# Performance work log

Measured on AMD Instinct MI355X. Metric: run time of the kernel, lower is better.

Reference implementation:

```python
import jax, jax.numpy as jnp
import numpy as np

VIOL_TOL = 12.0
CLASH_TOL = 1.5
C_N_LEN = (1.329, 1.341)        # (non-proline, proline)
C_N_STD = (0.014, 0.016)
CA_C_N = (-0.5203, 0.0353)      # (gt cos, stddev)
C_N_CA = (-0.4473, 0.0311)
EPS = 1e-6


def setup_inputs() -> dict:
    key = jax.random.key(0)
    k = jax.random.split(key, 6)
    B, N = 1, 512
    pos = jax.random.normal(k[0], (B, N, 14, 3), jnp.float32) * 5.0
    atom_mask = jnp.ones((B, N, 14), jnp.float32)
    residue_types = jax.random.randint(k[1], (B, N), 0, 21, dtype=jnp.int32)
    residue_index = jnp.broadcast_to(jnp.arange(N, dtype=jnp.int32)[None], (B, N))
    vdw_table = jax.random.uniform(k[2], (21, 14), jnp.float32, 1.0, 2.0)
    lower_bound_table = jax.random.uniform(k[3], (21, 14, 14), jnp.float32, 1.0, 2.0)
    upper_bound_table = lower_bound_table + jax.random.uniform(k[4], (21, 14, 14), jnp.float32, 0.5, 1.5)
    return {
        'predicted_positions': pos,
        'atom_mask': atom_mask,
        'residue_types': residue_types,
        'residue_index': residue_index,
        'vdw_table': vdw_table,
        'lower_bound_table': lower_bound_table,
        'upper_bound_table': upper_bound_table,
    }


def _bond_angle_losses(pos, atom_mask, residue_types, residue_index):
    f32 = pos.dtype
    this_ca, this_ca_m = pos[:, :-1, 1, :], atom_mask[:, :-1, 1]
    this_c, this_c_m = pos[:, :-1, 2, :], atom_mask[:, :-1, 2]
    next_n, next_n_m = pos[:, 1:, 0, :], atom_mask[:, 1:, 0]
    next_ca, next_ca_m = pos[:, 1:, 1, :], atom_mask[:, 1:, 1]
    no_gap = (residue_index[:, 1:] - residue_index[:, :-1] == 1).astype(f32)

    c_n_len = jnp.sqrt(jnp.sum((this_c - next_n) ** 2, -1) + EPS)
    pro = (residue_types[:, 1:] == 14).astype(f32)
    gt_len = (1.0 - pro) * C_N_LEN[0] + pro * C_N_LEN[1]
    gt_std = (1.0 - pro) * C_N_STD[0] + pro * C_N_STD[1]
    c_n_mask = this_c_m * next_n_m * no_gap
    c_n_err = jnp.sqrt((c_n_len - gt_len) ** 2 + EPS)
    c_n_loss = jnp.sum(c_n_mask * jax.nn.relu(c_n_err - VIOL_TOL * gt_std), -1) / (jnp.sum(c_n_mask, -1) + EPS)

    ca_c_len = jnp.sqrt(jnp.sum((this_ca - this_c) ** 2, -1) + EPS)
    n_ca_len = jnp.sqrt(jnp.sum((next_n - next_ca) ** 2, -1) + EPS)
    c_ca_u = (this_ca - this_c) / ca_c_len[..., None]
    c_n_u = (next_n - this_c) / c_n_len[..., None]
    n_ca_u = (next_ca - next_n) / n_ca_len[..., None]

    ca_c_n = jnp.sum(c_ca_u * c_n_u, -1)
    ca_c_n_mask = this_ca_m * this_c_m * next_n_m * no_gap
    ca_c_n_err = jnp.sqrt((ca_c_n - CA_C_N[0]) ** 2 + EPS)
    ca_c_n_loss = jnp.sum(ca_c_n_mask * jax.nn.relu(ca_c_n_err - VIOL_TOL * CA_C_N[1]), -1) / (jnp.sum(ca_c_n_mask, -1) + EPS)

    c_n_ca = jnp.sum(-c_n_u * n_ca_u, -1)
    c_n_ca_mask = this_c_m * next_n_m * next_ca_m * no_gap
    c_n_ca_err = jnp.sqrt((c_n_ca - C_N_CA[0]) ** 2 + EPS)
    c_n_ca_loss = jnp.sum(c_n_ca_mask * jax.nn.relu(c_n_ca_err - VIOL_TOL * C_N_CA[1]), -1) / (jnp.sum(c_n_ca_mask, -1) + EPS)

    return c_n_loss, ca_c_n_loss, c_n_ca_loss


def _clash_per_atom(pos, atom_mask, residue_types, residue_index, vdw_table):
    f32 = pos.dtype
    B, N = pos.shape[:2]
    A = N * 14
    pos_f = pos.reshape(B, A, 3)
    m_f = atom_mask.reshape(B, A)
    rt = jnp.minimum(residue_types, 20)
    vdw_f = vdw_table[rt].reshape(B, A)  # gather [B,N,14] -> flat

    diff = pos_f[:, :, None, :] - pos_f[:, None, :, :]
    dist = jnp.sqrt(jnp.sum(diff ** 2, -1) + 1e-8)  # [B,A,A]

    pair = m_f[:, :, None] * m_f[:, None, :]
    ari = jnp.repeat(residue_index, 14, axis=1)  # atom residue index [B,A]
    pair = pair * (ari[:, :, None] < ari[:, None, :]).astype(f32)

    slot = jnp.tile(jnp.arange(14), N)[None]  # [1,A]
    rtf = jnp.repeat(residue_types, 14, axis=1)
    c_n_bond = ((slot[:, :, None] == 2) & (slot[:, None, :] == 0) & (ari[:, None, :] - ari[:, :, None] == 1)) | \
               ((slot[:, :, None] == 0) & (slot[:, None, :] == 2) & (ari[:, :, None] - ari[:, None, :] == 1))
    disulfide = (rtf[:, :, None] == 4) & (rtf[:, None, :] == 4) & (slot[:, :, None] == 5) & (slot[:, None, :] == 5)
    pair = pair * (~c_n_bond).astype(f32) * (~disulfide).astype(f32)

    vdw_sum = vdw_f[:, :, None] + vdw_f[:, None, :]
    clash = jax.nn.relu(vdw_sum - CLASH_TOL - dist) * pair
    per_atom = (jnp.sum(clash, axis=1) + jnp.sum(clash, axis=2)).reshape(B, N, 14)
    return per_atom


def _within_per_atom(pos, atom_mask, residue_types, lower_bound_table, upper_bound_table):
    f32 = pos.dtype
    rt = jnp.minimum(residue_types, 20)
    lb = lower_bound_table[rt]  # [B,N,14,14]
    ub = upper_bound_table[rt]
    d = jnp.sqrt(jnp.sum((pos[:, :, :, None, :] - pos[:, :, None, :, :]) ** 2, -1) + 1e-8)
    pair = atom_mask[:, :, :, None] * atom_mask[:, :, None, :]
    pair = pair * (1.0 - jnp.eye(14, dtype=f32)[None, None])
    pair = pair * ((lb > 0.0) | (ub > 0.0)).astype(f32)
    loss = (jax.nn.relu(lb - d) + jax.nn.relu(d - ub)) * pair
    return jnp.sum(loss, axis=-2) + jnp.sum(loss, axis=-1)  # [B,N,14]


def reference(predicted_positions, atom_mask, residue_types, residue_index,
              vdw_table, lower_bound_table, upper_bound_table):
    c_n, ca_c_n, c_n_ca = _bond_angle_losses(predicted_positions, atom_mask, residue_types, residue_index)
    clash_pa = _clash_per_atom(predicted_positions, atom_mask, residue_types, residue_index, vdw_table)
    within_pa = _within_per_atom(predicted_positions, atom_mask, residue_types, lower_bound_table, upper_bound_table)
    num_atoms = jnp.clip(jnp.sum(atom_mask, axis=(1, 2)), 1e-6, None)
    clash_loss = jnp.sum(clash_pa + within_pa, axis=(1, 2)) / num_atoms
    return c_n + ca_c_n + c_n_ca + clash_loss
```

## Files before the change

### kernel.cpp

```cpp
#include <hip/hip_runtime.h>

#define EPS 1e-6f
#define JT 128
#define WB 64

static __device__ __forceinline__ float wave_reduce_add(float v) {
#pragma unroll
    for (int o = 32; o > 0; o >>= 1) v += __shfl_down(v, o, 64);
    return v;
}


__device__ void do_bonds(const float* __restrict__ P, const float* __restrict__ M,
                         const int* __restrict__ RT, const int* __restrict__ RI,
                         float* __restrict__ W, int N) {
    float n0 = 0.f, de0 = 0.f, n1 = 0.f, de1 = 0.f, n2 = 0.f, de2 = 0.f;
    for (int i = threadIdx.x; i < N - 1; i += blockDim.x) {
        float no_gap = (RI[i + 1] - RI[i] == 1) ? 1.f : 0.f;
        const float* ca0 = P + i * 42 + 3;
        const float* c0  = P + i * 42 + 6;
        const float* nn  = P + (i + 1) * 42 + 0;
        const float* ca1 = P + (i + 1) * 42 + 3;
        float m_ca0 = M[i * 14 + 1], m_c0 = M[i * 14 + 2];
        float m_nn = M[(i + 1) * 14 + 0], m_ca1 = M[(i + 1) * 14 + 1];

        float bx = nn[0] - c0[0], by = nn[1] - c0[1], bz = nn[2] - c0[2];
        float c_n_len = sqrtf(bx * bx + by * by + bz * bz + EPS);
        float pro = (RT[i + 1] == 14) ? 1.f : 0.f;
        float gt_len = (1.f - pro) * 1.329f + pro * 1.341f;
        float gt_std = (1.f - pro) * 0.014f + pro * 0.016f;
        float cnm = m_c0 * m_nn * no_gap;
        float dl = c_n_len - gt_len;
        float cne = sqrtf(dl * dl + EPS);
        n0 += cnm * fmaxf(cne - 12.f * gt_std, 0.f);
        de0 += cnm;

        float ax = ca0[0] - c0[0], ay = ca0[1] - c0[1], az = ca0[2] - c0[2];
        float ca_c_len = sqrtf(ax * ax + ay * ay + az * az + EPS);
        float ex = ca1[0] - nn[0], ey = ca1[1] - nn[1], ez = ca1[2] - nn[2];
        float n_ca_len = sqrtf(ex * ex + ey * ey + ez * ez + EPS);
        float inv_cn = 1.f / c_n_len, inv_ac = 1.f / ca_c_len, inv_nc = 1.f / n_ca_len;
        float ux = bx * inv_cn, uy = by * inv_cn, uz = bz * inv_cn;
        float cx = ax * inv_ac, cy = ay * inv_ac, cz = az * inv_ac;
        float wx = ex * inv_nc, wy = ey * inv_nc, wz = ez * inv_nc;

        float cacn = cx * ux + cy * uy + cz * uz;
        float m1 = m_ca0 * m_c0 * m_nn * no_gap;
        float t1 = cacn + 0.5203f;
        float e1 = sqrtf(t1 * t1 + EPS);
        n1 += m1 * fmaxf(e1 - 12.f * 0.0353f, 0.f);
        de1 += m1;

        float cnca = -(ux * wx + uy * wy + uz * wz);
        float m2 = m_c0 * m_nn * m_ca1 * no_gap;
        float t2 = cnca + 0.4473f;
        float e2 = sqrtf(t2 * t2 + EPS);
        n2 += m2 * fmaxf(e2 - 12.f * 0.0311f, 0.f);
        de2 += m2;
    }
    n0 = wave_reduce_add(n0); de0 = wave_reduce_add(de0);
    n1 = wave_reduce_add(n1); de1 = wave_reduce_add(de1);
    n2 = wave_reduce_add(n2); de2 = wave_reduce_add(de2);
    __shared__ float red[12];
    int lane = threadIdx.x & 63, wid = threadIdx.x >> 6;
    if (lane == 0) {
        red[wid * 6 + 0] = n0; red[wid * 6 + 1] = de0; red[wid * 6 + 2] = n1;
        red[wid * 6 + 3] = de1; red[wid * 6 + 4] = n2; red[wid * 6 + 5] = de2;
    }
    __syncthreads();
    if (threadIdx.x == 0) {
        atomicAdd(&W[0], red[0] + red[6]); atomicAdd(&W[1], red[1] + red[7]);
        atomicAdd(&W[2], red[2] + red[8]); atomicAdd(&W[3], red[3] + red[9]);
        atomicAdd(&W[4], red[4] + red[10]); atomicAdd(&W[5], red[5] + red[11]);
    }
}

__device__ void do_within(const float* __restrict__ pos, const float* __restrict__ am,
                          const int* __restrict__ rtypes,
                          const float* __restrict__ lbt, const float* __restrict__ ubt,
                          float* __restrict__ W, int N, int b, int wblk) {
    int total = N * 196;
    float sum = 0.f;
    for (int idx = wblk * blockDim.x + threadIdx.x; idx < total; idx += WB * blockDim.x) {
        int n = idx / 196;
        int p = idx - n * 196;
        int i = p / 14;
        int j = p - i * 14;
        if (i == j) continue;
        size_t bn = (size_t)b * N + n;
        int rt = rtypes[bn]; rt = rt < 20 ? rt : 20;
        const float* pi = pos + bn * 42 + i * 3;
        const float* pj = pos + bn * 42 + j * 3;
        float dx = pi[0] - pj[0], dy = pi[1] - pj[1], dz = pi[2] - pj[2];
        float d = sqrtf(dx * dx + dy * dy + dz * dz + 1e-8f);
        float lb = lbt[rt * 196 + p], ub = ubt[rt * 196 + p];
        float gate = (lb > 0.f || ub > 0.f) ? 1.f : 0.f;
        float m = am[bn * 14 + i] * am[bn * 14 + j] * gate;
        sum += (fmaxf(lb - d, 0.f) + fmaxf(d - ub, 0.f)) * m;
    }
    sum = wave_reduce_add(sum);
    __shared__ float red2[2];
    int lane = threadIdx.x & 63, wid = threadIdx.x >> 6;
    if (lane == 0) red2[wid] = sum;
    __syncthreads();
    if (threadIdx.x == 0) {
        float s = red2[0] + red2[1];
        if (s != 0.f) atomicAdd(&W[7], s);
    }
}

__device__ void do_clash(const float* __restrict__ P, const float* __restrict__ M,
                         const int* __restrict__ RT, const int* __restrict__ RI,
                         const float* __restrict__ vdw, float* __restrict__ W,
                         int N, int A, int T, int p) {
    int bi = (int)floorf(((float)(2 * T + 1)
                - sqrtf((float)((2 * T + 1) * (2 * T + 1) - 8 * p))) * 0.5f);
    bi = bi < 0 ? 0 : (bi >= T ? T - 1 : bi);
    while (bi + 1 <= T - 1 && ((bi + 1) * T - (bi + 1) * bi / 2) <= p) ++bi;
    while ((bi * T - bi * (bi - 1) / 2) > p) --bi;
    int bj = bi + (p - (bi * T - bi * (bi - 1) / 2));

    __shared__ float4 sPos[JT];
    __shared__ float sMask[JT];
    __shared__ int sRI[JT];
    __shared__ int sMeta[JT];

    int t = threadIdx.x;
    int j = bj * JT + t;
    if (j < A) {
        int res = j / 14;
        int sl = j - res * 14;
        int rt = RT[res];
        int rtc = rt < 20 ? rt : 20;
        sPos[t] = make_float4(P[j * 3], P[j * 3 + 1], P[j * 3 + 2], vdw[rtc * 14 + sl]);
        sMask[t] = M[j];
        sRI[t] = RI[res];
        sMeta[t] = sl | (((rt == 4) && (sl == 5)) ? 16 : 0);
    } else {
        sPos[t] = make_float4(1e30f, 1e30f, 1e30f, -1e30f);
        sMask[t] = 0.f; sRI[t] = 0x7fffffff; sMeta[t] = 0;
    }
    __syncthreads();

    int i = bi * JT + t;
    float sum = 0.f;
    if (i < A) {
        int res = i / 14;
        int isl = i - res * 14;
        int irt = RT[res];
        int rtc = irt < 20 ? irt : 20;
        float vis = vdw[rtc * 14 + isl] - 1.5f;
        float xi = P[i * 3], yi = P[i * 3 + 1], zi = P[i * 3 + 2];
        float mi = M[i];
        int iri = RI[res];
        bool icys = (irt == 4) && (isl == 5);
        if (mi != 0.f) {
            for (int base = 0; base < JT; base += 8) {
                float4 r[8];
#pragma unroll
                for (int k = 0; k < 8; ++k) r[k] = sPos[base + k];
#pragma unroll
                for (int k = 0; k < 8; ++k) {
                    float dx = xi - r[k].x, dy = yi - r[k].y, dz = zi - r[k].z;
                    float d2 = dx * dx + dy * dy + dz * dz + 1e-8f;
                    float s = vis + r[k].w;
                    if (d2 < s * s && s > 0.f) {
                        int jj = base + k;
                        int jg = bj * JT + jj;
                        if (i < jg) {
                            int jri = sRI[jj];
                            if (iri != jri) {
                                int dj = jri - iri;
                                int jmeta = sMeta[jj];
                                int jsl = jmeta & 15;
                                bool cn = (isl == 2 && jsl == 0 && dj == 1) ||
                                          (isl == 0 && jsl == 2 && dj == -1);
                                bool ssb = icys && (jmeta & 16);
                                if (!cn && !ssb) {
                                    sum += (s - sqrtf(d2)) * mi * sMask[jj];
                                }
                            }
                        }
                    }
                }
            }
        }
    }
    sum = wave_reduce_add(sum);
    __shared__ float red3[2];
    int lane = t & 63, wid = t >> 6;
    if (lane == 0) red3[wid] = sum;
    __syncthreads();
    if (t == 0) {
        float s = red3[0] + red3[1];
        if (s != 0.f) atomicAdd(&W[6], s);
    }
}

__global__ __launch_bounds__(JT) void main_kernel(
        const float* __restrict__ pos, const float* __restrict__ am,
        const int* __restrict__ rtypes, const int* __restrict__ rindex,
        const float* __restrict__ vdw, const float* __restrict__ lbt,
        const float* __restrict__ ubt, float* __restrict__ ws,
        int N, int A, int T, int CB) {
    int b = blockIdx.y;
    const float* P = pos + (size_t)b * A * 3;
    const float* M = am + (size_t)b * A;
    const int* RT = rtypes + (size_t)b * N;
    const int* RI = rindex + (size_t)b * N;
    float* W = ws + b * 8;
    int bid = blockIdx.x;
    if (bid < CB) {
        do_clash(P, M, RT, RI, vdw, W, N, A, T, bid);
    } else if (bid < CB + WB) {
        do_within(pos, am, rtypes, lbt, ubt, W, N, b, bid - CB);
    } else {
        do_bonds(P, M, RT, RI, W, N);
    }
}

__global__ __launch_bounds__(128) void final_kernel(
        const float* __restrict__ am, const float* __restrict__ ws,
        float* __restrict__ out, int N) {
    int b = blockIdx.x;
    const float* M = am + (size_t)b * N * 14;
    float s = 0.f;
    for (int i = threadIdx.x; i < N * 14; i += blockDim.x) s += M[i];
    s = wave_reduce_add(s);
    __shared__ float red[2];
    int lane = threadIdx.x & 63, wid = threadIdx.x >> 6;
    if (lane == 0) red[wid] = s;
    __syncthreads();
    if (threadIdx.x == 0) {
        float na = fmaxf(red[0] + red[1], 1e-6f);
        const float* W = ws + b * 8;
        float loss = W[0] / (W[1] + EPS) + W[2] / (W[3] + EPS) + W[4] / (W[5] + EPS)
                   + 2.f * (W[6] + W[7]) / na;
        out[b] = loss;
    }
}

extern "C" void kernel_launch(void* const* d_in, const int* in_sizes, int n_in,
                              void* d_out, int out_size, void* d_ws, size_t ws_size,
                              hipStream_t stream) {
    const float* pos = (const float*)d_in[0];
    const float* am = (const float*)d_in[1];
    const int* rtypes = (const int*)d_in[2];
    const int* rindex = (const int*)d_in[3];
    const float* vdw = (const float*)d_in[4];
    const float* lbt = (const float*)d_in[5];
    const float* ubt = (const float*)d_in[6];
    float* out = (float*)d_out;
    float* ws = (float*)d_ws;

    int B = out_size;
    int N = in_sizes[2] / B;
    int A = N * 14;
    int T = (A + JT - 1) / JT;
    int CB = T * (T + 1) / 2;

    hipMemsetAsync(ws, 0, (size_t)B * 8 * sizeof(float), stream);
    dim3 grid(CB + WB + 1, B);
    main_kernel<<<grid, JT, 0, stream>>>(pos, am, rtypes, rindex, vdw, lbt, ubt,
                                         ws, N, A, T, CB);
    final_kernel<<<B, 128, 0, stream>>>(am, ws, out, N);
}
```

Baseline: 106.0 us.

## Replace atomics and memset with per-block partial slots; enlarge clash tiles to 256

Each block now writes its partial sum into its own workspace slot instead of doing atomicAdd into shared accumulators, and the final kernel sums the slots, so the hipMemsetAsync launch can be dropped. The clash tile size and block size go from 128 to 256 threads, which quarters the number of triangular tile pairs, and the within-residue block count changes from 64 to 56. This removes a memset launch and atomic contention but makes the final reduction read more values and changes the load per block.

```diff
diff --git a/kernel.cpp b/kernel.cpp
--- a/kernel.cpp
+++ b/kernel.cpp
@@ -1,8 +1,8 @@
 #include <hip/hip_runtime.h>
 
 #define EPS 1e-6f
-#define JT 128
-#define WB 64
+#define JT 256
+#define WB 56
 
 static __device__ __forceinline__ float wave_reduce_add(float v) {
 #pragma unroll
@@ -13,7 +13,7 @@
 
 __device__ void do_bonds(const float* __restrict__ P, const float* __restrict__ M,
                          const int* __restrict__ RT, const int* __restrict__ RI,
-                         float* __restrict__ W, int N) {
+                         float* __restrict__ Wtail, int N) {
     float n0 = 0.f, de0 = 0.f, n1 = 0.f, de1 = 0.f, n2 = 0.f, de2 = 0.f;
     for (int i = threadIdx.x; i < N - 1; i += blockDim.x) {
         float no_gap = (RI[i + 1] - RI[i] == 1) ? 1.f : 0.f;
@@ -61,24 +61,23 @@
     n0 = wave_reduce_add(n0); de0 = wave_reduce_add(de0);
     n1 = wave_reduce_add(n1); de1 = wave_reduce_add(de1);
     n2 = wave_reduce_add(n2); de2 = wave_reduce_add(de2);
-    __shared__ float red[12];
+    __shared__ float red[24];
     int lane = threadIdx.x & 63, wid = threadIdx.x >> 6;
     if (lane == 0) {
         red[wid * 6 + 0] = n0; red[wid * 6 + 1] = de0; red[wid * 6 + 2] = n1;
         red[wid * 6 + 3] = de1; red[wid * 6 + 4] = n2; red[wid * 6 + 5] = de2;
     }
     __syncthreads();
-    if (threadIdx.x == 0) {
-        atomicAdd(&W[0], red[0] + red[6]); atomicAdd(&W[1], red[1] + red[7]);
-        atomicAdd(&W[2], red[2] + red[8]); atomicAdd(&W[3], red[3] + red[9]);
-        atomicAdd(&W[4], red[4] + red[10]); atomicAdd(&W[5], red[5] + red[11]);
+    if (threadIdx.x < 6) {
+        Wtail[threadIdx.x] = red[threadIdx.x] + red[6 + threadIdx.x]
+                           + red[12 + threadIdx.x] + red[18 + threadIdx.x];
     }
 }
 
 __device__ void do_within(const float* __restrict__ pos, const float* __restrict__ am,
                           const int* __restrict__ rtypes,
                           const float* __restrict__ lbt, const float* __restrict__ ubt,
-                          float* __restrict__ W, int N, int b, int wblk) {
+                          float* __restrict__ slot, int N, int b, int wblk) {
     int total = N * 196;
     float sum = 0.f;
     for (int idx = wblk * blockDim.x + threadIdx.x; idx < total; idx += WB * blockDim.x) {
@@ -99,19 +98,16 @@
         sum += (fmaxf(lb - d, 0.f) + fmaxf(d - ub, 0.f)) * m;
     }
     sum = wave_reduce_add(sum);
-    __shared__ float red2[2];
+    __shared__ float red2[4];
     int lane = threadIdx.x & 63, wid = threadIdx.x >> 6;
     if (lane == 0) red2[wid] = sum;
     __syncthreads();
-    if (threadIdx.x == 0) {
-        float s = red2[0] + red2[1];
-        if (s != 0.f) atomicAdd(&W[7], s);
-    }
+    if (threadIdx.x == 0) *slot = red2[0] + red2[1] + red2[2] + red2[3];
 }
 
 __device__ void do_clash(const float* __restrict__ P, const float* __restrict__ M,
                          const int* __restrict__ RT, const int* __restrict__ RI,
-                         const float* __restrict__ vdw, float* __restrict__ W,
+                         const float* __restrict__ vdw, float* __restrict__ slot,
                          int N, int A, int T, int p) {
     int bi = (int)floorf(((float)(2 * T + 1)
                 - sqrtf((float)((2 * T + 1) * (2 * T + 1) - 8 * p))) * 0.5f);
@@ -187,14 +183,11 @@
         }
     }
     sum = wave_reduce_add(sum);
-    __shared__ float red3[2];
+    __shared__ float red3[4];
     int lane = t & 63, wid = t >> 6;
     if (lane == 0) red3[wid] = sum;
     __syncthreads();
-    if (t == 0) {
-        float s = red3[0] + red3[1];
-        if (s != 0.f) atomicAdd(&W[6], s);
-    }
+    if (t == 0) *slot = red3[0] + red3[1] + red3[2] + red3[3];
 }
 
 __global__ __launch_bounds__(JT) void main_kernel(
@@ -202,40 +195,44 @@
         const int* __restrict__ rtypes, const int* __restrict__ rindex,
         const float* __restrict__ vdw, const float* __restrict__ lbt,
         const float* __restrict__ ubt, float* __restrict__ ws,
-        int N, int A, int T, int CB) {
+        int N, int A, int T, int CB, int NBP, int stride) {
     int b = blockIdx.y;
     const float* P = pos + (size_t)b * A * 3;
     const float* M = am + (size_t)b * A;
     const int* RT = rtypes + (size_t)b * N;
     const int* RI = rindex + (size_t)b * N;
-    float* W = ws + b * 8;
+    float* W = ws + (size_t)b * stride;
     int bid = blockIdx.x;
     if (bid < CB) {
-        do_clash(P, M, RT, RI, vdw, W, N, A, T, bid);
-    } else if (bid < CB + WB) {
-        do_within(pos, am, rtypes, lbt, ubt, W, N, b, bid - CB);
+        do_clash(P, M, RT, RI, vdw, &W[bid], N, A, T, bid);
+    } else if (bid < NBP) {
+        do_within(pos, am, rtypes, lbt, ubt, &W[bid], N, b, bid - CB);
     } else {
-        do_bonds(P, M, RT, RI, W, N);
-    }
-}
-
-__global__ __launch_bounds__(128) void final_kernel(
+        do_bonds(P, M, RT, RI, &W[NBP], N);
+    }
+}
+
+__global__ __launch_bounds__(256) void final_kernel(
         const float* __restrict__ am, const float* __restrict__ ws,
-        float* __restrict__ out, int N) {
+        float* __restrict__ out, int N, int NBP, int stride) {
     int b = blockIdx.x;
     const float* M = am + (size_t)b * N * 14;
-    float s = 0.f;
+    const float* W = ws + (size_t)b * stride;
+    float s = 0.f, pairs = 0.f;
     for (int i = threadIdx.x; i < N * 14; i += blockDim.x) s += M[i];
+    for (int i = threadIdx.x; i < NBP; i += blockDim.x) pairs += W[i];
     s = wave_reduce_add(s);
-    __shared__ float red[2];
+    pairs = wave_reduce_add(pairs);
+    __shared__ float red[8];
     int lane = threadIdx.x & 63, wid = threadIdx.x >> 6;
-    if (lane == 0) red[wid] = s;
+    if (lane == 0) { red[wid] = s; red[4 + wid] = pairs; }
     __syncthreads();
     if (threadIdx.x == 0) {
-        float na = fmaxf(red[0] + red[1], 1e-6f);
-        const float* W = ws + b * 8;
-        float loss = W[0] / (W[1] + EPS) + W[2] / (W[3] + EPS) + W[4] / (W[5] + EPS)
-                   + 2.f * (W[6] + W[7]) / na;
+        float na = fmaxf(red[0] + red[1] + red[2] + red[3], 1e-6f);
+        float P2 = red[4] + red[5] + red[6] + red[7];
+        const float* T6 = W + NBP;
+        float loss = T6[0] / (T6[1] + EPS) + T6[2] / (T6[3] + EPS)
+                   + T6[4] / (T6[5] + EPS) + 2.f * P2 / na;
         out[b] = loss;
     }
 }
@@ -258,10 +255,11 @@
     int A = N * 14;
     int T = (A + JT - 1) / JT;
     int CB = T * (T + 1) / 2;
-
-    hipMemsetAsync(ws, 0, (size_t)B * 8 * sizeof(float), stream);
-    dim3 grid(CB + WB + 1, B);
+    int NBP = CB + WB;
+    int stride = NBP + 6;
+
+    dim3 grid(NBP + 1, B);
     main_kernel<<<grid, JT, 0, stream>>>(pos, am, rtypes, rindex, vdw, lbt, ubt,
-                                         ws, N, A, T, CB);
-    final_kernel<<<B, 128, 0, stream>>>(am, ws, out, N);
-}
+                                         ws, N, A, T, CB, NBP, stride);
+    final_kernel<<<B, 256, 0, stream>>>(am, ws, out, N, NBP, stride);
+}
```

Result: faster. 101.9 us (-3.8%).
